# Kernel tuning notes

Hardware: AMD Instinct MI355X
Metric: run time of the kernel (lower is better)

## Reference

```python
import jax, jax.numpy as jnp
import numpy as np

DIM = 96
NUM_HEADS = 3
WINDOW = (2, 7, 7)


def _relative_position_index(ws):
    # same construction as the torch buffer, done once in numpy (static)
    wd, wh, ww = ws
    coords = np.stack(np.meshgrid(np.arange(wd), np.arange(wh), np.arange(ww), indexing='ij'))
    coords_flat = coords.reshape(3, -1)                      # [3, N]
    rel = coords_flat[:, :, None] - coords_flat[:, None, :]  # [3, N, N]
    rel = rel.transpose(1, 2, 0).astype(np.int64)            # [N, N, 3]
    rel[:, :, 0] += wd - 1
    rel[:, :, 1] += wh - 1
    rel[:, :, 2] += ww - 1
    rel[:, :, 0] *= (2 * wh - 1) * (2 * ww - 1)
    rel[:, :, 1] *= 2 * ww - 1
    return rel.sum(-1)                                       # [N, N]


def setup_inputs() -> dict:
    key = jax.random.key(0)
    ks = jax.random.split(key, 6)
    B_ = 4096
    N = WINDOW[0] * WINDOW[1] * WINDOW[2]  # 98
    C = DIM
    table_len = (2 * WINDOW[0] - 1) * (2 * WINDOW[1] - 1) * (2 * WINDOW[2] - 1)  # 507
    x = jax.random.normal(ks[0], (B_, N, C), dtype=jnp.float32)
    qkv_w = jax.random.normal(ks[1], (3 * C, C), dtype=jnp.float32) * (1.0 / np.sqrt(C))
    qkv_b = jnp.zeros((3 * C,), dtype=jnp.float32)
    proj_w = jax.random.normal(ks[2], (C, C), dtype=jnp.float32) * (1.0 / np.sqrt(C))
    proj_b = jnp.zeros((C,), dtype=jnp.float32)
    bias_table = jax.random.normal(ks[3], (table_len, NUM_HEADS), dtype=jnp.float32) * 0.02
    rel_index = jnp.asarray(_relative_position_index(WINDOW), dtype=jnp.int32)  # [N, N]
    return {"x": x, "qkv_w": qkv_w, "qkv_b": qkv_b, "proj_w": proj_w,
            "proj_b": proj_b, "bias_table": bias_table, "rel_index": rel_index}


def reference(x, qkv_w, qkv_b, proj_w, proj_b, bias_table, rel_index):
    B_, N, C = x.shape
    H = NUM_HEADS
    hd = C // H
    scale = hd ** (-0.5)
    qkv = x @ qkv_w.T + qkv_b                        # [B_, N, 3C]
    qkv = qkv.reshape(B_, N, 3, H, hd).transpose(2, 0, 3, 1, 4)  # [3, B_, H, N, hd]
    q, k, v = qkv[0], qkv[1], qkv[2]
    attn = jnp.einsum('bhnd,bhmd->bhnm', q, k) * scale           # [B_, H, N, N]
    bias = bias_table[rel_index.reshape(-1)].reshape(N, N, H).transpose(2, 0, 1)  # [H, N, N]
    attn = jax.nn.softmax(attn + bias[None], axis=-1)
    out = jnp.einsum('bhnm,bhmd->bhnd', attn, v)                 # [B_, H, N, hd]
    out = out.transpose(0, 2, 1, 3).reshape(B_, N, C)
    return out @ proj_w.T + proj_b
```

## Files before the change

kernel.cpp:

```cpp
#include <hip/hip_runtime.h>
#include <stdint.h>

#define NTOK 98
#define CDIM 96
#define LDK 104
#define LDV 120
#define LDSCR 40

typedef __bf16 bf16x8 __attribute__((ext_vector_type(8)));
typedef float f32x4 __attribute__((ext_vector_type(4)));

__device__ __forceinline__ uint16_t f2bfbits(float f) {
  uint32_t u = __builtin_bit_cast(uint32_t, f);
  u += 0x7FFFu + ((u >> 16) & 1u);
  return (uint16_t)(u >> 16);
}
__device__ __forceinline__ __bf16 bits2bf(uint16_t h) {
  return __builtin_bit_cast(__bf16, h);
}
__device__ __forceinline__ __bf16 f2bf(float f) { return bits2bf(f2bfbits(f)); }

__device__ __forceinline__ bf16x8 cvt8(const float* p) {
  float4 a = *(const float4*)p;
  float4 b = *(const float4*)(p + 4);
  bf16x8 r;
  r[0] = f2bf(a.x); r[1] = f2bf(a.y); r[2] = f2bf(a.z); r[3] = f2bf(a.w);
  r[4] = f2bf(b.x); r[5] = f2bf(b.y); r[6] = f2bf(b.z); r[7] = f2bf(b.w);
  return r;
}

__global__ void precompute(const float* __restrict__ qkv_w,
                           const float* __restrict__ proj_w,
                           const float* __restrict__ bias_table,
                           const int* __restrict__ rel_index,
                           uint16_t* __restrict__ qkv_wp,
                           uint16_t* __restrict__ proj_wp,
                           float* __restrict__ bias_full) {
  int t = blockIdx.x * blockDim.x + threadIdx.x;
  int stride = gridDim.x * blockDim.x;
  for (int f = t; f < 18 * 3 * 4 * 16 * 8; f += stride) {
    int j = f & 7, l16 = (f >> 3) & 15, quad = (f >> 7) & 3, ktnt = f >> 9;
    int kt = ktnt % 3, nt = ktnt / 3;
    qkv_wp[f] = f2bfbits(qkv_w[(nt * 16 + l16) * CDIM + kt * 32 + quad * 8 + j]);
  }
  for (int f = t; f < 6 * 3 * 4 * 16 * 8; f += stride) {
    int j = f & 7, l16 = (f >> 3) & 15, quad = (f >> 7) & 3, ktnt = f >> 9;
    int kt = ktnt % 3, nt = ktnt / 3;
    proj_wp[f] = f2bfbits(proj_w[(nt * 16 + l16) * CDIM + kt * 32 + quad * 8 + j]);
  }
  for (int f = t; f < 3 * 128 * 112; f += stride) {
    int col = f % 112;
    int hr = f / 112;
    int row = hr & 127;
    int h = hr >> 7;
    float v = 0.f;
    if (row < NTOK && col < NTOK)
      v = bias_table[rel_index[row * NTOK + col] * 3 + h];
    bias_full[f] = v;
  }
}

__global__ __launch_bounds__(256, 3) void wattn3d(
    const float* __restrict__ x, const float* __restrict__ qkv_b,
    const float* __restrict__ proj_b, const uint16_t* __restrict__ qkv_wp,
    const uint16_t* __restrict__ proj_wp, const float* __restrict__ bias_full,
    float* __restrict__ out) {
  __shared__ __align__(16) char smem[53664];
  __bf16* k_lds = (__bf16*)smem;
  __bf16* vT = (__bf16*)(smem + 20384);
  __bf16* scr = (__bf16*)(smem + 43424);

  const int tid = threadIdx.x;
  const int wave = tid >> 6;
  const int lane = tid & 63;
  const int quad = lane >> 4;
  const int l16 = lane & 15;
  const int b = blockIdx.x;
  const int rowbase = wave * 32;
  __bf16* myscr = &scr[wave * 32 * LDSCR];
  const float scale = 0.17677669529663687f;

  for (int i = tid; i < CDIM * 8; i += 256) {
    int d = i >> 3, tk = 112 + (i & 7);
    vT[d * LDV + tk] = bits2bf(0);
  }

  const float* xb = x + (size_t)b * NTOK * CDIM;

  bf16x8 a_x[2][3];
#pragma unroll
  for (int mt = 0; mt < 2; ++mt) {
    int row = rowbase + mt * 16 + l16;
#pragma unroll
    for (int kt = 0; kt < 3; ++kt) {
      if (row < NTOK) {
        a_x[mt][kt] = cvt8(xb + row * CDIM + kt * 32 + quad * 8);
      } else {
        bf16x8 z;
#pragma unroll
        for (int j = 0; j < 8; ++j) z[j] = bits2bf(0);
        a_x[mt][kt] = z;
      }
    }
  }

  uint32_t qreg[2][6][2];
#pragma unroll
  for (int nt = 0; nt < 18; ++nt) {
    bf16x8 bw[3];
#pragma unroll
    for (int kt = 0; kt < 3; ++kt)
      bw[kt] = *(const bf16x8*)(qkv_wp + (((nt * 3 + kt) * 4 + quad) * 16 + l16) * 8);
    float bn = qkv_b[nt * 16 + l16];
#pragma unroll
    for (int mt = 0; mt < 2; ++mt) {
      f32x4 acc = {0.f, 0.f, 0.f, 0.f};
#pragma unroll
      for (int kt = 0; kt < 3; ++kt)
        acc = __builtin_amdgcn_mfma_f32_16x16x32_bf16(a_x[mt][kt], bw[kt], acc, 0, 0, 0);
      if (nt < 6) {
        uint16_t h4[4];
#pragma unroll
        for (int i = 0; i < 4; ++i) h4[i] = f2bfbits((acc[i] + bn) * scale);
        qreg[mt][nt][0] = (uint32_t)h4[0] | ((uint32_t)h4[1] << 16);
        qreg[mt][nt][1] = (uint32_t)h4[2] | ((uint32_t)h4[3] << 16);
      } else if (nt < 12) {
        int colb = (nt - 6) * 16 + l16;
#pragma unroll
        for (int i = 0; i < 4; ++i) {
          int row = rowbase + mt * 16 + quad * 4 + i;
          if (row < NTOK) k_lds[row * LDK + colb] = f2bf(acc[i] + bn);
        }
      } else {
        int d = (nt - 12) * 16 + l16;
        int t0 = rowbase + mt * 16 + quad * 4;
        if (t0 < 112) {
          uint16_t h4[4];
#pragma unroll
          for (int i = 0; i < 4; ++i) h4[i] = f2bfbits(acc[i] + bn);
          uint2 pk;
          pk.x = (uint32_t)h4[0] | ((uint32_t)h4[1] << 16);
          pk.y = (uint32_t)h4[2] | ((uint32_t)h4[3] << 16);
          *(uint2*)&vT[d * LDV + t0] = pk;
        }
      }
    }
  }
  __syncthreads();

  float rsum[2][4];
  f32x4 oacc[2][2];

#pragma unroll
  for (int h = 0; h < 3; ++h) {
#pragma unroll
    for (int mt = 0; mt < 2; ++mt)
#pragma unroll
      for (int nth = 0; nth < 2; ++nth) {
        uint32_t w0 = qreg[mt][2 * h + nth][0];
        uint32_t w1 = qreg[mt][2 * h + nth][1];
        int lr = mt * 16 + quad * 4;
        int cc = nth * 16 + l16;
        myscr[(lr + 0) * LDSCR + cc] = bits2bf((uint16_t)(w0 & 0xffffu));
        myscr[(lr + 1) * LDSCR + cc] = bits2bf((uint16_t)(w0 >> 16));
        myscr[(lr + 2) * LDSCR + cc] = bits2bf((uint16_t)(w1 & 0xffffu));
        myscr[(lr + 3) * LDSCR + cc] = bits2bf((uint16_t)(w1 >> 16));
      }
    asm volatile("s_waitcnt lgkmcnt(0)" ::: "memory");
    bf16x8 aq[2];
#pragma unroll
    for (int mt = 0; mt < 2; ++mt)
      aq[mt] = *(bf16x8*)&myscr[(mt * 16 + l16) * LDSCR + quad * 8];

    f32x4 sacc[2][7];
#pragma unroll
    for (int nt = 0; nt < 7; ++nt) {
      int tok = nt * 16 + l16;
      bf16x8 bk = *(bf16x8*)&k_lds[tok * LDK + h * 32 + quad * 8];
#pragma unroll
      for (int mt = 0; mt < 2; ++mt) {
        f32x4 z = {0.f, 0.f, 0.f, 0.f};
        sacc[mt][nt] = __builtin_amdgcn_mfma_f32_16x16x32_bf16(aq[mt], bk, z, 0, 0, 0);
      }
    }

#pragma unroll
    for (int mt = 0; mt < 2; ++mt)
#pragma unroll
      for (int i = 0; i < 4; ++i) {
        int row = rowbase + mt * 16 + quad * 4 + i;
        float mx = -1e30f;
#pragma unroll
        for (int nt = 0; nt < 7; ++nt) {
          int col = nt * 16 + l16;
          float s = (col < NTOK)
                        ? sacc[mt][nt][i] + bias_full[(h * 128 + row) * 112 + col]
                        : -1e30f;
          sacc[mt][nt][i] = s;
          mx = fmaxf(mx, s);
        }
#pragma unroll
        for (int d2 = 1; d2 < 16; d2 <<= 1) mx = fmaxf(mx, __shfl_xor(mx, d2));
        float sum = 0.f;
#pragma unroll
        for (int nt = 0; nt < 7; ++nt) {
          float p = __expf(sacc[mt][nt][i] - mx);
          sacc[mt][nt][i] = p;
          sum += p;
        }
#pragma unroll
        for (int d2 = 1; d2 < 16; d2 <<= 1) sum += __shfl_xor(sum, d2);
        rsum[mt][i] = 1.f / sum;
      }

#pragma unroll
    for (int mt = 0; mt < 2; ++mt)
#pragma unroll
      for (int nh = 0; nh < 2; ++nh) {
        f32x4 z = {0.f, 0.f, 0.f, 0.f};
        oacc[mt][nh] = z;
      }
#pragma unroll
    for (int kt2 = 0; kt2 < 4; ++kt2) {
#pragma unroll
      for (int half = 0; half < 2; ++half) {
        int ntS = 2 * kt2 + half;
#pragma unroll
        for (int mt = 0; mt < 2; ++mt) {
          int lr = mt * 16 + quad * 4;
          int cc = half * 16 + l16;
#pragma unroll
          for (int i = 0; i < 4; ++i) {
            float v = (ntS < 7) ? sacc[mt][ntS][i] : 0.f;
            myscr[(lr + i) * LDSCR + cc] = f2bf(v);
          }
        }
      }
      asm volatile("s_waitcnt lgkmcnt(0)" ::: "memory");
#pragma unroll
      for (int mt = 0; mt < 2; ++mt) {
        bf16x8 ap = *(bf16x8*)&myscr[(mt * 16 + l16) * LDSCR + quad * 8];
#pragma unroll
        for (int nh = 0; nh < 2; ++nh) {
          bf16x8 bv = *(bf16x8*)&vT[(h * 32 + nh * 16 + l16) * LDV + kt2 * 32 + quad * 8];
          oacc[mt][nh] = __builtin_amdgcn_mfma_f32_16x16x32_bf16(ap, bv, oacc[mt][nh], 0, 0, 0);
        }
      }
    }

    __syncthreads();
#pragma unroll
    for (int mt = 0; mt < 2; ++mt)
#pragma unroll
      for (int nh = 0; nh < 2; ++nh)
#pragma unroll
        for (int i = 0; i < 4; ++i) {
          int row = rowbase + mt * 16 + quad * 4 + i;
          if (row < NTOK)
            k_lds[row * LDK + h * 32 + nh * 16 + l16] =
                f2bf(oacc[mt][nh][i] * rsum[mt][i]);
        }
  }

  bf16x8 ao[2][3];
#pragma unroll
  for (int mt = 0; mt < 2; ++mt) {
    int arow = rowbase + mt * 16 + l16;
    if (arow >= 112) arow = 0;
#pragma unroll
    for (int kt = 0; kt < 3; ++kt)
      ao[mt][kt] = *(bf16x8*)&k_lds[arow * LDK + kt * 32 + quad * 8];
  }
  float* outb = out + (size_t)b * NTOK * CDIM;
#pragma unroll
  for (int nt = 0; nt < 6; ++nt) {
    bf16x8 bp[3];
#pragma unroll
    for (int kt = 0; kt < 3; ++kt)
      bp[kt] = *(const bf16x8*)(proj_wp + (((nt * 3 + kt) * 4 + quad) * 16 + l16) * 8);
    float pb = proj_b[nt * 16 + l16];
#pragma unroll
    for (int mt = 0; mt < 2; ++mt) {
      f32x4 acc = {0.f, 0.f, 0.f, 0.f};
#pragma unroll
      for (int kt = 0; kt < 3; ++kt)
        acc = __builtin_amdgcn_mfma_f32_16x16x32_bf16(ao[mt][kt], bp[kt], acc, 0, 0, 0);
#pragma unroll
      for (int i = 0; i < 4; ++i) {
        int row = rowbase + mt * 16 + quad * 4 + i;
        if (row < NTOK) outb[row * CDIM + nt * 16 + l16] = acc[i] + pb;
      }
    }
  }
}

extern "C" void kernel_launch(void* const* d_in, const int* in_sizes, int n_in,
                              void* d_out, int out_size, void* d_ws, size_t ws_size,
                              hipStream_t stream) {
  (void)n_in; (void)out_size; (void)ws_size;
  const float* x = (const float*)d_in[0];
  const float* qkv_w = (const float*)d_in[1];
  const float* qkv_b = (const float*)d_in[2];
  const float* proj_w = (const float*)d_in[3];
  const float* proj_b = (const float*)d_in[4];
  const float* bias_table = (const float*)d_in[5];
  const int* rel_index = (const int*)d_in[6];
  float* out = (float*)d_out;

  uint16_t* qkv_wp = (uint16_t*)d_ws;
  uint16_t* proj_wp = (uint16_t*)((char*)d_ws + 55296);
  float* bias_full = (float*)((char*)d_ws + 73728);

  precompute<<<dim3(64), dim3(256), 0, stream>>>(qkv_w, proj_w, bias_table,
                                                 rel_index, qkv_wp, proj_wp,
                                                 bias_full);
  int Bwin = in_sizes[0] / (NTOK * CDIM);
  wattn3d<<<dim3(Bwin), dim3(256), 0, stream>>>(x, qkv_b, proj_b, qkv_wp,
                                                proj_wp, bias_full, out);
}
```

Baseline: 446.6 us.

## Keep Q, P and O in registers via transposed MFMA and ds_bpermute rechunking

Q, the softmax probabilities and the attention output now stay in registers. The score and PV products are computed in transposed orientation, so each lane owns one query row, and ds_bpermute reshuffles accumulator fragments into MFMA operand layout. This removes the per-wave LDS scratch round-trips and s_waitcnt stalls, the end-of-head __syncthreads and the k_lds write-back of O. It also cuts shared memory, and softmax reductions need only two cross-lane shuffles instead of four. Other changes are float4 bias and output stores and hardware bf16 conversion. The cost is extra bpermute traffic and higher register pressure.

```diff
diff --git a/kernel.cpp b/kernel.cpp
--- a/kernel.cpp
+++ b/kernel.cpp
@@ -5,9 +5,9 @@
 #define CDIM 96
 #define LDK 104
 #define LDV 120
-#define LDSCR 40
 
 typedef __bf16 bf16x8 __attribute__((ext_vector_type(8)));
+typedef __bf16 bf16x2 __attribute__((ext_vector_type(2)));
 typedef float f32x4 __attribute__((ext_vector_type(4)));
 
 __device__ __forceinline__ uint16_t f2bfbits(float f) {
@@ -15,18 +15,40 @@
   u += 0x7FFFu + ((u >> 16) & 1u);
   return (uint16_t)(u >> 16);
 }
-__device__ __forceinline__ __bf16 bits2bf(uint16_t h) {
-  return __builtin_bit_cast(__bf16, h);
-}
-__device__ __forceinline__ __bf16 f2bf(float f) { return bits2bf(f2bfbits(f)); }
+
+__device__ __forceinline__ uint32_t pk2(float a, float b) {
+  bf16x2 t;
+  t[0] = (__bf16)a;
+  t[1] = (__bf16)b;
+  return __builtin_bit_cast(uint32_t, t);
+}
 
 __device__ __forceinline__ bf16x8 cvt8(const float* p) {
   float4 a = *(const float4*)p;
   float4 b = *(const float4*)(p + 4);
   bf16x8 r;
-  r[0] = f2bf(a.x); r[1] = f2bf(a.y); r[2] = f2bf(a.z); r[3] = f2bf(a.w);
-  r[4] = f2bf(b.x); r[5] = f2bf(b.y); r[6] = f2bf(b.z); r[7] = f2bf(b.w);
+  r[0] = (__bf16)a.x; r[1] = (__bf16)a.y; r[2] = (__bf16)a.z; r[3] = (__bf16)a.w;
+  r[4] = (__bf16)b.x; r[5] = (__bf16)b.y; r[6] = (__bf16)b.z; r[7] = (__bf16)b.w;
   return r;
+}
+
+__device__ __forceinline__ bf16x8 rechunk(uint32_t e0, uint32_t e1, uint32_t o0,
+                                          uint32_t o1, int selA, int selB,
+                                          bool lowq) {
+  int a0 = __builtin_amdgcn_ds_bpermute(selA, (int)e0);
+  int a1 = __builtin_amdgcn_ds_bpermute(selA, (int)e1);
+  int b0 = __builtin_amdgcn_ds_bpermute(selB, (int)e0);
+  int b1 = __builtin_amdgcn_ds_bpermute(selB, (int)e1);
+  int a0o = __builtin_amdgcn_ds_bpermute(selA, (int)o0);
+  int a1o = __builtin_amdgcn_ds_bpermute(selA, (int)o1);
+  int b0o = __builtin_amdgcn_ds_bpermute(selB, (int)o0);
+  int b1o = __builtin_amdgcn_ds_bpermute(selB, (int)o1);
+  uint4 w;
+  w.x = (uint32_t)(lowq ? a0 : a0o);
+  w.y = (uint32_t)(lowq ? a1 : a1o);
+  w.z = (uint32_t)(lowq ? b0 : b0o);
+  w.w = (uint32_t)(lowq ? b1 : b1o);
+  return __builtin_bit_cast(bf16x8, w);
 }
 
 __global__ void precompute(const float* __restrict__ qkv_w,
@@ -65,10 +87,9 @@
     const float* __restrict__ proj_b, const uint16_t* __restrict__ qkv_wp,
     const uint16_t* __restrict__ proj_wp, const float* __restrict__ bias_full,
     float* __restrict__ out) {
-  __shared__ __align__(16) char smem[53664];
+  __shared__ __align__(16) char smem[43552];
   __bf16* k_lds = (__bf16*)smem;
   __bf16* vT = (__bf16*)(smem + 20384);
-  __bf16* scr = (__bf16*)(smem + 43424);
 
   const int tid = threadIdx.x;
   const int wave = tid >> 6;
@@ -77,13 +98,17 @@
   const int l16 = lane & 15;
   const int b = blockIdx.x;
   const int rowbase = wave * 32;
-  __bf16* myscr = &scr[wave * 32 * LDSCR];
   const float scale = 0.17677669529663687f;
+
+  const int selA = (l16 | (((2 * quad) & 3) << 4)) << 2;
+  const int selB = (l16 | (((2 * quad + 1) & 3) << 4)) << 2;
+  const bool lowq = quad < 2;
 
   for (int i = tid; i < CDIM * 8; i += 256) {
     int d = i >> 3, tk = 112 + (i & 7);
-    vT[d * LDV + tk] = bits2bf(0);
-  }
+    vT[d * LDV + tk] = (__bf16)0.0f;
+  }
+  if (tid < 32) ((uint32_t*)(smem + 43424))[tid] = 0u;
 
   const float* xb = x + (size_t)b * NTOK * CDIM;
 
@@ -98,15 +123,33 @@
       } else {
         bf16x8 z;
 #pragma unroll
-        for (int j = 0; j < 8; ++j) z[j] = bits2bf(0);
+        for (int j = 0; j < 8; ++j) z[j] = (__bf16)0.0f;
         a_x[mt][kt] = z;
       }
     }
   }
 
-  uint32_t qreg[2][6][2];
-#pragma unroll
-  for (int nt = 0; nt < 18; ++nt) {
+  uint32_t qpk[2][6][2];
+#pragma unroll
+  for (int nt = 0; nt < 6; ++nt) {
+    bf16x8 bw[3];
+#pragma unroll
+    for (int kt = 0; kt < 3; ++kt)
+      bw[kt] = *(const bf16x8*)(qkv_wp + (((nt * 3 + kt) * 4 + quad) * 16 + l16) * 8);
+    float4 qb4 = *(const float4*)&qkv_b[nt * 16 + quad * 4];
+#pragma unroll
+    for (int mt = 0; mt < 2; ++mt) {
+      f32x4 acc = {0.f, 0.f, 0.f, 0.f};
+#pragma unroll
+      for (int kt = 0; kt < 3; ++kt)
+        acc = __builtin_amdgcn_mfma_f32_16x16x32_bf16(bw[kt], a_x[mt][kt], acc, 0, 0, 0);
+      qpk[mt][nt][0] = pk2((acc[0] + qb4.x) * scale, (acc[1] + qb4.y) * scale);
+      qpk[mt][nt][1] = pk2((acc[2] + qb4.z) * scale, (acc[3] + qb4.w) * scale);
+    }
+  }
+
+#pragma unroll
+  for (int nt = 6; nt < 18; ++nt) {
     bf16x8 bw[3];
 #pragma unroll
     for (int kt = 0; kt < 3; ++kt)
@@ -118,29 +161,20 @@
 #pragma unroll
       for (int kt = 0; kt < 3; ++kt)
         acc = __builtin_amdgcn_mfma_f32_16x16x32_bf16(a_x[mt][kt], bw[kt], acc, 0, 0, 0);
-      if (nt < 6) {
-        uint16_t h4[4];
-#pragma unroll
-        for (int i = 0; i < 4; ++i) h4[i] = f2bfbits((acc[i] + bn) * scale);
-        qreg[mt][nt][0] = (uint32_t)h4[0] | ((uint32_t)h4[1] << 16);
-        qreg[mt][nt][1] = (uint32_t)h4[2] | ((uint32_t)h4[3] << 16);
-      } else if (nt < 12) {
+      if (nt < 12) {
         int colb = (nt - 6) * 16 + l16;
 #pragma unroll
         for (int i = 0; i < 4; ++i) {
           int row = rowbase + mt * 16 + quad * 4 + i;
-          if (row < NTOK) k_lds[row * LDK + colb] = f2bf(acc[i] + bn);
+          if (row < NTOK) k_lds[row * LDK + colb] = (__bf16)(acc[i] + bn);
         }
       } else {
         int d = (nt - 12) * 16 + l16;
         int t0 = rowbase + mt * 16 + quad * 4;
         if (t0 < 112) {
-          uint16_t h4[4];
-#pragma unroll
-          for (int i = 0; i < 4; ++i) h4[i] = f2bfbits(acc[i] + bn);
           uint2 pk;
-          pk.x = (uint32_t)h4[0] | ((uint32_t)h4[1] << 16);
-          pk.y = (uint32_t)h4[2] | ((uint32_t)h4[3] << 16);
+          pk.x = pk2(acc[0] + bn, acc[1] + bn);
+          pk.y = pk2(acc[2] + bn, acc[3] + bn);
           *(uint2*)&vT[d * LDV + t0] = pk;
         }
       }
@@ -148,71 +182,63 @@
   }
   __syncthreads();
 
-  float rsum[2][4];
-  f32x4 oacc[2][2];
+  uint32_t opk[2][3][4];
+  float rs[2];
 
 #pragma unroll
   for (int h = 0; h < 3; ++h) {
+    bf16x8 qf[2];
 #pragma unroll
     for (int mt = 0; mt < 2; ++mt)
-#pragma unroll
-      for (int nth = 0; nth < 2; ++nth) {
-        uint32_t w0 = qreg[mt][2 * h + nth][0];
-        uint32_t w1 = qreg[mt][2 * h + nth][1];
-        int lr = mt * 16 + quad * 4;
-        int cc = nth * 16 + l16;
-        myscr[(lr + 0) * LDSCR + cc] = bits2bf((uint16_t)(w0 & 0xffffu));
-        myscr[(lr + 1) * LDSCR + cc] = bits2bf((uint16_t)(w0 >> 16));
-        myscr[(lr + 2) * LDSCR + cc] = bits2bf((uint16_t)(w1 & 0xffffu));
-        myscr[(lr + 3) * LDSCR + cc] = bits2bf((uint16_t)(w1 >> 16));
-      }
-    asm volatile("s_waitcnt lgkmcnt(0)" ::: "memory");
-    bf16x8 aq[2];
-#pragma unroll
-    for (int mt = 0; mt < 2; ++mt)
-      aq[mt] = *(bf16x8*)&myscr[(mt * 16 + l16) * LDSCR + quad * 8];
+      qf[mt] = rechunk(qpk[mt][2 * h][0], qpk[mt][2 * h][1],
+                       qpk[mt][2 * h + 1][0], qpk[mt][2 * h + 1][1],
+                       selA, selB, lowq);
 
     f32x4 sacc[2][7];
 #pragma unroll
     for (int nt = 0; nt < 7; ++nt) {
-      int tok = nt * 16 + l16;
-      bf16x8 bk = *(bf16x8*)&k_lds[tok * LDK + h * 32 + quad * 8];
+      bf16x8 ak = *(bf16x8*)&k_lds[(nt * 16 + l16) * LDK + h * 32 + quad * 8];
 #pragma unroll
       for (int mt = 0; mt < 2; ++mt) {
         f32x4 z = {0.f, 0.f, 0.f, 0.f};
-        sacc[mt][nt] = __builtin_amdgcn_mfma_f32_16x16x32_bf16(aq[mt], bk, z, 0, 0, 0);
-      }
-    }
-
-#pragma unroll
-    for (int mt = 0; mt < 2; ++mt)
-#pragma unroll
-      for (int i = 0; i < 4; ++i) {
-        int row = rowbase + mt * 16 + quad * 4 + i;
-        float mx = -1e30f;
-#pragma unroll
-        for (int nt = 0; nt < 7; ++nt) {
-          int col = nt * 16 + l16;
-          float s = (col < NTOK)
-                        ? sacc[mt][nt][i] + bias_full[(h * 128 + row) * 112 + col]
-                        : -1e30f;
+        sacc[mt][nt] = __builtin_amdgcn_mfma_f32_16x16x32_bf16(ak, qf[mt], z, 0, 0, 0);
+      }
+    }
+
+#pragma unroll
+    for (int mt = 0; mt < 2; ++mt) {
+      const int qrow = rowbase + mt * 16 + l16;
+      const float* brow = bias_full + ((size_t)h * 128 + qrow) * 112 + quad * 4;
+      float mx = -1e30f;
+#pragma unroll
+      for (int nt = 0; nt < 7; ++nt) {
+        float4 b4 = *(const float4*)(brow + nt * 16);
+        float bv[4] = {b4.x, b4.y, b4.z, b4.w};
+#pragma unroll
+        for (int i = 0; i < 4; ++i) {
+          float s = sacc[mt][nt][i] + bv[i];
+          if (nt == 6 && !(quad == 0 && i < 2)) s = -1e30f;
           sacc[mt][nt][i] = s;
           mx = fmaxf(mx, s);
         }
-#pragma unroll
-        for (int d2 = 1; d2 < 16; d2 <<= 1) mx = fmaxf(mx, __shfl_xor(mx, d2));
-        float sum = 0.f;
-#pragma unroll
-        for (int nt = 0; nt < 7; ++nt) {
+      }
+      mx = fmaxf(mx, __shfl_xor(mx, 16));
+      mx = fmaxf(mx, __shfl_xor(mx, 32));
+      float sum = 0.f;
+#pragma unroll
+      for (int nt = 0; nt < 7; ++nt)
+#pragma unroll
+        for (int i = 0; i < 4; ++i) {
           float p = __expf(sacc[mt][nt][i] - mx);
           sacc[mt][nt][i] = p;
           sum += p;
         }
-#pragma unroll
-        for (int d2 = 1; d2 < 16; d2 <<= 1) sum += __shfl_xor(sum, d2);
-        rsum[mt][i] = 1.f / sum;
-      }
-
+      sum += __shfl_xor(sum, 16);
+      sum += __shfl_xor(sum, 32);
+      rs[mt] = 1.f / sum;
+    }
+
+    f32x4 oacc[2][2];
 #pragma unroll
     for (int mt = 0; mt < 2; ++mt)
 #pragma unroll
@@ -222,73 +248,61 @@
       }
 #pragma unroll
     for (int kt2 = 0; kt2 < 4; ++kt2) {
-#pragma unroll
-      for (int half = 0; half < 2; ++half) {
-        int ntS = 2 * kt2 + half;
-#pragma unroll
-        for (int mt = 0; mt < 2; ++mt) {
-          int lr = mt * 16 + quad * 4;
-          int cc = half * 16 + l16;
-#pragma unroll
-          for (int i = 0; i < 4; ++i) {
-            float v = (ntS < 7) ? sacc[mt][ntS][i] : 0.f;
-            myscr[(lr + i) * LDSCR + cc] = f2bf(v);
-          }
-        }
-      }
-      asm volatile("s_waitcnt lgkmcnt(0)" ::: "memory");
+      bf16x8 av[2];
+#pragma unroll
+      for (int nh = 0; nh < 2; ++nh)
+        av[nh] = *(bf16x8*)&vT[(h * 32 + nh * 16 + l16) * LDV + kt2 * 32 + quad * 8];
 #pragma unroll
       for (int mt = 0; mt < 2; ++mt) {
-        bf16x8 ap = *(bf16x8*)&myscr[(mt * 16 + l16) * LDSCR + quad * 8];
-#pragma unroll
-        for (int nh = 0; nh < 2; ++nh) {
-          bf16x8 bv = *(bf16x8*)&vT[(h * 32 + nh * 16 + l16) * LDV + kt2 * 32 + quad * 8];
-          oacc[mt][nh] = __builtin_amdgcn_mfma_f32_16x16x32_bf16(ap, bv, oacc[mt][nh], 0, 0, 0);
-        }
-      }
-    }
-
-    __syncthreads();
-#pragma unroll
-    for (int mt = 0; mt < 2; ++mt)
-#pragma unroll
-      for (int nh = 0; nh < 2; ++nh)
-#pragma unroll
-        for (int i = 0; i < 4; ++i) {
-          int row = rowbase + mt * 16 + quad * 4 + i;
-          if (row < NTOK)
-            k_lds[row * LDK + h * 32 + nh * 16 + l16] =
-                f2bf(oacc[mt][nh][i] * rsum[mt][i]);
-        }
-  }
-
-  bf16x8 ao[2][3];
+        uint32_t e0 = pk2(sacc[mt][2 * kt2][0], sacc[mt][2 * kt2][1]);
+        uint32_t e1 = pk2(sacc[mt][2 * kt2][2], sacc[mt][2 * kt2][3]);
+        uint32_t o0 = 0u, o1 = 0u;
+        if (kt2 < 3) {
+          o0 = pk2(sacc[mt][2 * kt2 + 1][0], sacc[mt][2 * kt2 + 1][1]);
+          o1 = pk2(sacc[mt][2 * kt2 + 1][2], sacc[mt][2 * kt2 + 1][3]);
+        }
+        bf16x8 pf = rechunk(e0, e1, o0, o1, selA, selB, lowq);
+#pragma unroll
+        for (int nh = 0; nh < 2; ++nh)
+          oacc[mt][nh] = __builtin_amdgcn_mfma_f32_16x16x32_bf16(av[nh], pf, oacc[mt][nh], 0, 0, 0);
+      }
+    }
+
+#pragma unroll
+    for (int mt = 0; mt < 2; ++mt) {
+      float r = rs[mt];
+      opk[mt][h][0] = pk2(oacc[mt][0][0] * r, oacc[mt][0][1] * r);
+      opk[mt][h][1] = pk2(oacc[mt][0][2] * r, oacc[mt][0][3] * r);
+      opk[mt][h][2] = pk2(oacc[mt][1][0] * r, oacc[mt][1][1] * r);
+      opk[mt][h][3] = pk2(oacc[mt][1][2] * r, oacc[mt][1][3] * r);
+    }
+  }
+
+  float* outb = out + (size_t)b * NTOK * CDIM;
 #pragma unroll
   for (int mt = 0; mt < 2; ++mt) {
-    int arow = rowbase + mt * 16 + l16;
-    if (arow >= 112) arow = 0;
+    bf16x8 of[3];
 #pragma unroll
     for (int kt = 0; kt < 3; ++kt)
-      ao[mt][kt] = *(bf16x8*)&k_lds[arow * LDK + kt * 32 + quad * 8];
-  }
-  float* outb = out + (size_t)b * NTOK * CDIM;
-#pragma unroll
-  for (int nt = 0; nt < 6; ++nt) {
-    bf16x8 bp[3];
-#pragma unroll
-    for (int kt = 0; kt < 3; ++kt)
-      bp[kt] = *(const bf16x8*)(proj_wp + (((nt * 3 + kt) * 4 + quad) * 16 + l16) * 8);
-    float pb = proj_b[nt * 16 + l16];
-#pragma unroll
-    for (int mt = 0; mt < 2; ++mt) {
+      of[kt] = rechunk(opk[mt][kt][0], opk[mt][kt][1], opk[mt][kt][2],
+                       opk[mt][kt][3], selA, selB, lowq);
+    const int qrow = rowbase + mt * 16 + l16;
+#pragma unroll
+    for (int nt = 0; nt < 6; ++nt) {
       f32x4 acc = {0.f, 0.f, 0.f, 0.f};
 #pragma unroll
-      for (int kt = 0; kt < 3; ++kt)
-        acc = __builtin_amdgcn_mfma_f32_16x16x32_bf16(ao[mt][kt], bp[kt], acc, 0, 0, 0);
-#pragma unroll
-      for (int i = 0; i < 4; ++i) {
-        int row = rowbase + mt * 16 + quad * 4 + i;
-        if (row < NTOK) outb[row * CDIM + nt * 16 + l16] = acc[i] + pb;
+      for (int kt = 0; kt < 3; ++kt) {
+        bf16x8 aw = *(const bf16x8*)(proj_wp + (((nt * 3 + kt) * 4 + quad) * 16 + l16) * 8);
+        acc = __builtin_amdgcn_mfma_f32_16x16x32_bf16(aw, of[kt], acc, 0, 0, 0);
+      }
+      if (qrow < NTOK) {
+        float4 pb4 = *(const float4*)&proj_b[nt * 16 + quad * 4];
+        float4 o4;
+        o4.x = acc[0] + pb4.x;
+        o4.y = acc[1] + pb4.y;
+        o4.z = acc[2] + pb4.z;
+        o4.w = acc[3] + pb4.w;
+        *(float4*)&outb[(size_t)qrow * CDIM + nt * 16 + quad * 4] = o4;
       }
     }
   }
```

Result: faster. 390.5 us (-12.6%).
